# Optimization experiments

Measured on AMD Instinct MI355X. Metric: run time of the kernel, lower is better.

Reference implementation:

```python
import jax, jax.numpy as jnp
import numpy as np
import math

NUM_HEADS = 16
SEGMENT_SIZE = 256
DILATION_RATE = 2


def _hilbert_curve(n):
    if n == 1:
        return [(0, 0)]
    m = n // 2
    sub = _hilbert_curve(m)
    pts = [(y, x) for (x, y) in sub]
    pts += [(x, y + m) for (x, y) in sub]
    pts += [(x + m, y + m) for (x, y) in sub]
    pts += [(m - 1 - y + m, m - 1 - x) for (x, y) in sub]
    return pts


def generate_hilbert_curve_mapping(seq_len):
    grid = 2 ** int(math.ceil(math.log2(math.sqrt(seq_len))))
    pts = _hilbert_curve(grid)
    lin2hil = np.zeros(seq_len, dtype=np.int32)
    for h_idx, (x, y) in enumerate(pts[:seq_len]):
        lin = y * grid + x
        if lin < seq_len:
            lin2hil[lin] = h_idx
    return lin2hil


def setup_inputs() -> dict:
    key = jax.random.key(0)
    k1, k2, k3 = jax.random.split(key, 3)
    B, S, H = 1, 4096, 2048
    scale = H ** -0.5
    x = jax.random.normal(k1, (B, S, H), dtype=jnp.float32)
    w_qkv = jax.random.normal(k2, (3 * H, H), dtype=jnp.float32) * scale
    w_out = jax.random.normal(k3, (H, H), dtype=jnp.float32) * scale
    hilbert_map = jnp.asarray(generate_hilbert_curve_mapping(S))
    return {"x": x, "w_qkv": w_qkv, "w_out": w_out, "hilbert_map": hilbert_map}


def _kv_positions(S, seg, dil):
    # Union of per-segment dilated positions: seg_start + j*dil (< segment end).
    seg_starts = np.arange(0, S, seg)
    within = np.arange(0, seg, dil)
    return jnp.asarray((seg_starts[:, None] + within[None, :]).reshape(-1))


def reference(x, w_qkv, w_out, hilbert_map):
    B, S, H = x.shape
    nh = NUM_HEADS
    hd = H // nh
    qkv = x @ w_qkv.T                              # [B,S,3H]
    qkv = qkv.reshape(B, S, 3, nh, hd).transpose(2, 0, 3, 1, 4)  # [3,B,nh,S,hd]
    q, k, v = qkv[0], qkv[1], qkv[2]

    kv_pos = _kv_positions(S, SEGMENT_SIZE, DILATION_RATE)  # [Nk]
    gathered = hilbert_map[kv_pos]                 # Hilbert-mapped KV indices
    kg = k[:, :, gathered, :]                      # [B,nh,Nk,hd]
    vg = v[:, :, gathered, :]

    scale = 1.0 / jnp.sqrt(jnp.float32(hd))
    scores = jnp.einsum("bhmd,bhnd->bhmn", q, kg) * scale
    p = jax.nn.softmax(scores, axis=-1)
    acc = jnp.einsum("bhmn,bhnd->bhmd", p, vg)     # [B,nh,S,hd]

    # Scatter: out[:, :, hilbert_map[m], :] = acc[:, :, m, :]
    out = jnp.zeros_like(acc).at[:, :, hilbert_map, :].set(acc)
    out = out.transpose(0, 2, 1, 3).reshape(B, S, H)
    return out @ w_out.T
```

## Files before the change

### kernel.cpp

```cpp
#include <hip/hip_runtime.h>
#include <math.h>

#define S_LEN 4096
#define HID   2048
#define NH    16
#define HD    128
#define NKV   2048
#define KT    64
#define QBLK  256
#define NT    (NKV / KT)
#define QSCALE 0.12754103668587426f

typedef __attribute__((ext_vector_type(8))) _Float16 half8;
typedef __attribute__((ext_vector_type(4))) _Float16 half4;
typedef __attribute__((ext_vector_type(2))) __fp16 fp16x2;
typedef __attribute__((ext_vector_type(4))) float f32x4;
typedef __attribute__((ext_vector_type(16))) float f32x16;

#define GLB_AS __attribute__((address_space(1)))
#define LDS_AS __attribute__((address_space(3)))

#if __has_builtin(__builtin_amdgcn_exp2f)
#define EXP2(x) __builtin_amdgcn_exp2f(x)
#else
#define EXP2(x) exp2f(x)
#endif

__device__ __forceinline__ void gload16(const void* g, void* l) {
  __builtin_amdgcn_global_load_lds((GLB_AS const void*)g, (LDS_AS void*)l, 16, 0, 0);
}

__device__ __forceinline__ unsigned pkrtz(float a, float b) {
  union { fp16x2 h; unsigned u; } cv;
  cv.h = __builtin_amdgcn_cvt_pkrtz(a, b);
  return cv.u;
}

__global__ void k_build_idx(const int* __restrict__ hmap, int* __restrict__ gidx) {
  int i = blockIdx.x * 256 + threadIdx.x;
  if (i < NKV) gidx[i] = hmap[2 * i];
}

#define NX8  (S_LEN * HID / 8)
#define NW8  (3 * HID * HID / 8)
#define NO8  (HID * HID / 8)
__global__ void k_cvt_all(const float* __restrict__ x, const float* __restrict__ wq,
                          const float* __restrict__ wo, _Float16* __restrict__ x16,
                          _Float16* __restrict__ wq16, _Float16* __restrict__ wo16) {
  int i = blockIdx.x * 256 + threadIdx.x;
  const float* src; _Float16* dst; int j;
  if (i < NX8)            { src = x;  dst = x16;  j = i; }
  else if (i < NX8 + NW8) { src = wq; dst = wq16; j = i - NX8; }
  else                    { src = wo; dst = wo16; j = i - NX8 - NW8; }
  float4 a = ((const float4*)src)[2 * j];
  float4 b = ((const float4*)src)[2 * j + 1];
  half8 h;
  h[0] = (_Float16)a.x; h[1] = (_Float16)a.y; h[2] = (_Float16)a.z; h[3] = (_Float16)a.w;
  h[4] = (_Float16)b.x; h[5] = (_Float16)b.y; h[6] = (_Float16)b.z; h[7] = (_Float16)b.w;
  ((half8*)dst)[j] = h;
}

template<int MODE>
__global__ __launch_bounds__(256)
void k_gemm2(const _Float16* __restrict__ A, const _Float16* __restrict__ B,
             void* __restrict__ Cv, int M, int N, int K,
             const int* __restrict__ arow,
             char* __restrict__ kimg, char* __restrict__ vtimg)
{
  __shared__ __align__(16) char Asl[16384];
  __shared__ __align__(16) char Bsl[16384];
  const int tid = threadIdx.x;
  const int w = tid >> 6, lane = tid & 63;
  const int l15 = lane & 15, l4 = lane >> 4;
  const int m0 = blockIdx.y * 128, n0 = blockIdx.x * 128;
  const int wr = w >> 1, wc = w & 1;

  const int srow  = lane >> 3;
  const int kso   = ((lane & 7) ^ srow) * 8;
  const _Float16* Ap[4];
  const _Float16* Bp[4];
#pragma unroll
  for (int q = 0; q < 4; ++q) {
    int arel = m0 + 32 * w + 8 * q + srow;
    int ra = arow ? arow[arel] : arel;
    Ap[q] = A + (size_t)ra * K + kso;
    Bp[q] = B + (size_t)(n0 + 32 * w + 8 * q + srow) * K + kso;
  }

  f32x4 acc[4][4];
#pragma unroll
  for (int i = 0; i < 4; ++i)
#pragma unroll
    for (int j = 0; j < 4; ++j) acc[i][j] = (f32x4){0.f, 0.f, 0.f, 0.f};

#define STAGE_T(k0)                                                  \
  do {                                                               \
    _Pragma("unroll")                                                \
    for (int q = 0; q < 4; ++q) {                                    \
      gload16(Ap[q] + (k0), Asl + (4 * w + q) * 1024 + lane * 16);   \
      gload16(Bp[q] + (k0), Bsl + (4 * w + q) * 1024 + lane * 16);   \
    }                                                                \
  } while (0)

  STAGE_T(0);
  __syncthreads();

  const int nt = K >> 6;
  for (int t = 0; t < nt; ++t) {
    half8 af[4][2], bf[4][2];
#pragma unroll
    for (int mi = 0; mi < 4; ++mi) {
      int row = wr * 64 + mi * 16 + l15;
#pragma unroll
      for (int ks = 0; ks < 2; ++ks)
        af[mi][ks] = *(const half8*)(Asl + row * 128 + (((ks * 4 + l4) ^ (row & 7)) * 16));
    }
#pragma unroll
    for (int ni = 0; ni < 4; ++ni) {
      int row = wc * 64 + ni * 16 + l15;
#pragma unroll
      for (int ks = 0; ks < 2; ++ks)
        bf[ni][ks] = *(const half8*)(Bsl + row * 128 + (((ks * 4 + l4) ^ (row & 7)) * 16));
    }
    __syncthreads();
    if (t + 1 < nt) STAGE_T((t + 1) * 64);
    __builtin_amdgcn_s_setprio(1);
#pragma unroll
    for (int mi = 0; mi < 4; ++mi)
#pragma unroll
      for (int ni = 0; ni < 4; ++ni)
#pragma unroll
        for (int ks = 0; ks < 2; ++ks)
          acc[mi][ni] = __builtin_amdgcn_mfma_f32_16x16x32_f16(af[mi][ks], bf[ni][ks], acc[mi][ni], 0, 0, 0);
    __builtin_amdgcn_s_setprio(0);
    __syncthreads();
  }
#undef STAGE_T

  const int rbase = m0 + wr * 64 + l4 * 4;
  const int cbase = n0 + wc * 64 + l15;
#pragma unroll
  for (int mi = 0; mi < 4; ++mi)
#pragma unroll
    for (int ni = 0; ni < 4; ++ni)
#pragma unroll
      for (int e = 0; e < 4; ++e) {
        int row = rbase + mi * 16 + e;
        int col = cbase + ni * 16;
        if (MODE == 1) {
          ((float*)Cv)[(size_t)row * N + col] = acc[mi][ni][e];
        } else if (MODE == 0) {
          ((_Float16*)Cv)[(size_t)row * N + col] = (_Float16)acc[mi][ni][e];
        } else {
          _Float16 val = (_Float16)acc[mi][ni][e];
          int t = row >> 6, j = row & 63;
          if (col < HID) {
            int h = col >> 7, d = col & 127;
            int off = (h * 32 + t) * 16384 + ((j * 256 + 2 * d) ^ ((j & 7) << 4));
            *(_Float16*)(kimg + off) = val;
          } else {
            int nn = col - HID;
            int h = nn >> 7, d = nn & 127;
            int off = (h * 32 + t) * 16384 + ((d * 128 + 2 * j) ^ ((d & 7) << 4));
            *(_Float16*)(vtimg + off) = val;
          }
        }
      }
}

__global__ __launch_bounds__(512, 2)
void k_attn9(const _Float16* __restrict__ qmat, const char* __restrict__ kimg,
             const char* __restrict__ vtimg, const int* __restrict__ hmap,
             _Float16* __restrict__ att)
{
  extern __shared__ __align__(16) char lds[];
  const int tid = threadIdx.x;
  const int w = tid >> 6, lane = tid & 63;
  const int l31 = lane & 31;
  const bool hi = (lane >> 5) != 0;
  const int hib = hi ? 1 : 0;
  const int work = (blockIdx.x & 7) * 32 + (blockIdx.x >> 3);
  const int h  = work >> 4;
  const int q0 = (work & 15) * QBLK;

  half8 qf[8];
  {
    const int qrow = q0 + w * 32 + l31;
    const _Float16* qb = qmat + (size_t)qrow * HID + h * HD + hib * 8;
    const _Float16 qs = (_Float16)QSCALE;
#pragma unroll
    for (int dk = 0; dk < 8; ++dk) {
      half8 v = *(const half8*)(qb + 16 * dk);
#pragma unroll
      for (int q = 0; q < 8; ++q) v[q] *= qs;
      qf[dk] = v;
    }
  }

  const int swz = (l31 & 7) << 4;
  int koff[4], voff[4];
#pragma unroll
  for (int i = 0; i < 4; ++i) {
    koff[i] = l31 * 256 + ((i * 32 + hib * 16) ^ swz);
    voff[i] = 16384 + l31 * 128 + ((i * 32 + hib * 16) ^ swz);
  }

  const char* kbase = kimg  + (size_t)h * NT * 16384;
  const char* vbase = vtimg + (size_t)h * NT * 16384;

  f32x16 acc[4];
#pragma unroll
  for (int dt = 0; dt < 4; ++dt)
#pragma unroll
    for (int r = 0; r < 16; ++r) acc[dt][r] = 0.f;
  float lsum = 0.f;

#define STAGE(buf, t)                                                          \
  do {                                                                         \
    const char* ks_ = kbase + (size_t)(t) * 16384;                             \
    const char* vs_ = vbase + (size_t)(t) * 16384;                             \
    char* d_ = lds + (buf) * 32768;                                            \
    gload16(ks_ + w * 1024 + lane * 16,          d_ + w * 1024);               \
    gload16(ks_ + (8 + w) * 1024 + lane * 16,    d_ + (8 + w) * 1024);         \
    gload16(vs_ + w * 1024 + lane * 16,          d_ + 16384 + w * 1024);       \
    gload16(vs_ + (8 + w) * 1024 + lane * 16,    d_ + 16384 + (8 + w) * 1024); \
  } while (0)

#define SM_HALF(S, PPK)                                                        \
  do {                                                                         \
    float p_[16];                                                              \
    _Pragma("unroll")                                                          \
    for (int r = 0; r < 16; ++r) { p_[r] = EXP2((S)[r]); lsum += p_[r]; }      \
    _Pragma("unroll")                                                          \
    for (int rq = 0; rq < 4; ++rq)                                             \
      _Pragma("unroll")                                                        \
      for (int h2 = 0; h2 < 2; ++h2)                                           \
        PPK[rq][h2] = pkrtz(p_[4 * rq + 2 * h2], p_[4 * rq + 2 * h2 + 1]);     \
  } while (0)

#define PV_HALF(PPK, KSB, CUR)                                                 \
  do {                                                                         \
    _Pragma("unroll")                                                          \
    for (int k1 = 0; k1 < 2; ++k1) {                                           \
      unsigned send0 = hi ? PPK[2 * k1][0]     : PPK[2 * k1 + 1][0];           \
      unsigned send1 = hi ? PPK[2 * k1][1]     : PPK[2 * k1 + 1][1];           \
      unsigned recv0 = (unsigned)__shfl_xor((int)send0, 32);                   \
      unsigned recv1 = (unsigned)__shfl_xor((int)send1, 32);                   \
      unsigned self0 = hi ? PPK[2 * k1 + 1][0] : PPK[2 * k1][0];               \
      unsigned self1 = hi ? PPK[2 * k1 + 1][1] : PPK[2 * k1][1];               \
      union { unsigned u[4]; half8 hv; } pf;                                   \
      pf.u[0] = hi ? recv0 : self0;                                            \
      pf.u[1] = hi ? recv1 : self1;                                            \
      pf.u[2] = hi ? self0 : recv0;                                            \
      pf.u[3] = hi ? self1 : recv1;                                            \
      __builtin_amdgcn_s_setprio(1);                                           \
      _Pragma("unroll")                                                        \
      for (int dt = 0; dt < 4; ++dt) {                                         \
        half8 vf = *(const half8*)(lds + voff[(KSB) + k1] +                    \
                    ((CUR) * 32768 + dt * 4096));                              \
        acc[dt] = __builtin_amdgcn_mfma_f32_32x32x16_f16(vf, pf.hv, acc[dt], 0, 0, 0); \
      }                                                                        \
      __builtin_amdgcn_s_setprio(0);                                           \
    }                                                                          \
  } while (0)

#define QK_HALF(S, JT, CUR)                                                    \
  do {                                                                         \
    _Pragma("unroll")                                                          \
    for (int r = 0; r < 16; ++r) (S)[r] = 0.f;                                 \
    __builtin_amdgcn_s_setprio(1);                                             \
    _Pragma("unroll")                                                          \
    for (int dk = 0; dk < 8; ++dk) {                                           \
      half8 kf = *(const half8*)(lds + koff[dk & 3] +                          \
                  ((CUR) * 32768 + (JT) * 8192 + (dk >> 2) * 128));            \
      (S) = __builtin_amdgcn_mfma_f32_32x32x16_f16(kf, qf[dk], (S), 0, 0, 0);  \
    }                                                                          \
    __builtin_amdgcn_s_setprio(0);                                             \
  } while (0)

#define TILE(CUR, T)                                                           \
  do {                                                                         \
    if ((T) + 1 < NT) STAGE((CUR) ^ 1, (T) + 1);                               \
    f32x16 sA, sB;                                                             \
    QK_HALF(sA, 0, CUR);                                                       \
    QK_HALF(sB, 1, CUR);                                                       \
    unsigned PA[4][2], PB[4][2];                                               \
    SM_HALF(sA, PA);                         \
    PV_HALF(PA, 0, CUR);                                                       \
    SM_HALF(sB, PB);                    \
    PV_HALF(PB, 2, CUR);                                                       \
    asm volatile("s_waitcnt vmcnt(0)");                                        \
    __syncthreads();                                                           \
  } while (0)

  STAGE(0, 0);
  asm volatile("s_waitcnt vmcnt(0)");
  __syncthreads();

  for (int t = 0; t < NT; t += 2) {
    TILE(0, t);
    TILE(1, t + 1);
  }
#undef TILE
#undef QK_HALF
#undef PV_HALF
#undef SM_HALF
#undef STAGE

  float lt = lsum + __shfl_xor(lsum, 32);
  const float rl = 1.0f / lt;
  const int qrow = q0 + w * 32 + l31;
  const int srow = hmap[qrow];
  _Float16* ob = att + (size_t)srow * HID + h * HD;
#pragma unroll
  for (int dt = 0; dt < 4; ++dt)
#pragma unroll
    for (int rq = 0; rq < 4; ++rq) {
      const int d0 = dt * 32 + 8 * rq + 4 * hib;
      half4 o;
      o[0] = (_Float16)(acc[dt][4 * rq + 0] * rl);
      o[1] = (_Float16)(acc[dt][4 * rq + 1] * rl);
      o[2] = (_Float16)(acc[dt][4 * rq + 2] * rl);
      o[3] = (_Float16)(acc[dt][4 * rq + 3] * rl);
      *(half4*)(ob + d0) = o;
    }
}

extern "C" void kernel_launch(void* const* d_in, const int* in_sizes, int n_in,
                              void* d_out, int out_size, void* d_ws, size_t ws_size,
                              hipStream_t stream)
{
  const float* x     = (const float*)d_in[0];
  const float* w_qkv = (const float*)d_in[1];
  const float* w_out = (const float*)d_in[2];
  const int*   hmap  = (const int*)d_in[3];
  float* out = (float*)d_out;

  char* ws = (char*)d_ws;
  int* gidx = (int*)ws;                                          ws += 8192;
  _Float16* x16    = (_Float16*)ws;
  _Float16* att16  = (_Float16*)ws;                              ws += (size_t)S_LEN * HID * 2;
  _Float16* wqkv16 = (_Float16*)ws;                              ws += (size_t)3 * HID * HID * 2;
  _Float16* wout16 = (_Float16*)ws;                              ws += (size_t)HID * HID * 2;
  _Float16* q16    = (_Float16*)ws;                              ws += (size_t)S_LEN * HID * 2;
  char* kimg  = ws;                                              ws += (size_t)NH * NT * 16384;
  char* vtimg = ws;

  k_build_idx<<<8, 256, 0, stream>>>(hmap, gidx);
  k_cvt_all<<<(NX8 + NW8 + NO8 + 255) / 256, 256, 0, stream>>>(x, w_qkv, w_out,
                                                               x16, wqkv16, wout16);

  dim3 gq(HID / 128, S_LEN / 128);
  k_gemm2<0><<<gq, 256, 0, stream>>>(x16, wqkv16, q16, S_LEN, HID, HID, nullptr, nullptr, nullptr);
  dim3 gkv(2 * HID / 128, NKV / 128);
  k_gemm2<2><<<gkv, 256, 0, stream>>>(x16, wqkv16 + (size_t)HID * HID, nullptr,
                                      NKV, 2 * HID, HID, gidx, kimg, vtimg);

  k_attn9<<<NH * (S_LEN / QBLK), 512, 65536, stream>>>(q16, kimg, vtimg, hmap, att16);

  dim3 go(HID / 128, S_LEN / 128);
  k_gemm2<1><<<go, 256, 0, stream>>>(att16, wout16, out, S_LEN, HID, HID, nullptr, nullptr, nullptr);
}
```

Baseline: 217.9 us.

## Merge Q and KV projection GEMMs into one launch; halve attention query block

The Q projection and the gathered K/V projection GEMMs now run as a single 1024-block launch, with the block index choosing which part it computes. This removes one kernel launch and lets both parts share the GPU at once, filling the tail. The attention kernel drops from 256 to 128 query rows per block and from 512 to 256 threads, doubling the number of blocks to 512. The trade-off is that each K/V tile staged in LDS is reused by fewer query rows, so more K/V traffic is loaded per unit of work. The output GEMM becomes its own non-templated kernel.

```diff
diff --git a/kernel.cpp b/kernel.cpp
--- a/kernel.cpp
+++ b/kernel.cpp
@@ -7,7 +7,7 @@
 #define HD    128
 #define NKV   2048
 #define KT    64
-#define QBLK  256
+#define QBLK  128
 #define NT    (NKV / KT)
 #define QSCALE 0.12754103668587426f
 
@@ -60,20 +60,27 @@
   ((half8*)dst)[j] = h;
 }
 
-template<int MODE>
 __global__ __launch_bounds__(256)
-void k_gemm2(const _Float16* __restrict__ A, const _Float16* __restrict__ B,
-             void* __restrict__ Cv, int M, int N, int K,
-             const int* __restrict__ arow,
-             char* __restrict__ kimg, char* __restrict__ vtimg)
+void k_gemm_qkv(const _Float16* __restrict__ A, const _Float16* __restrict__ wqkv,
+                _Float16* __restrict__ q16, const int* __restrict__ gidx,
+                char* __restrict__ kimg, char* __restrict__ vtimg)
 {
   __shared__ __align__(16) char Asl[16384];
   __shared__ __align__(16) char Bsl[16384];
   const int tid = threadIdx.x;
   const int w = tid >> 6, lane = tid & 63;
   const int l15 = lane & 15, l4 = lane >> 4;
-  const int m0 = blockIdx.y * 128, n0 = blockIdx.x * 128;
   const int wr = w >> 1, wc = w & 1;
+  const int K = HID;
+
+  int b = blockIdx.x;
+  const bool qpart = b < 512;
+  int m0, n0, N;
+  const _Float16* B;
+  const int* arow;
+  if (qpart) { m0 = (b >> 4) * 128; n0 = (b & 15) * 128; N = HID; B = wqkv; arow = nullptr; }
+  else { b -= 512; m0 = (b >> 5) * 128; n0 = (b & 31) * 128; N = 2 * HID;
+         B = wqkv + (size_t)HID * HID; arow = gidx; }
 
   const int srow  = lane >> 3;
   const int kso   = ((lane & 7) ^ srow) * 8;
@@ -147,12 +154,10 @@
       for (int e = 0; e < 4; ++e) {
         int row = rbase + mi * 16 + e;
         int col = cbase + ni * 16;
-        if (MODE == 1) {
-          ((float*)Cv)[(size_t)row * N + col] = acc[mi][ni][e];
-        } else if (MODE == 0) {
-          ((_Float16*)Cv)[(size_t)row * N + col] = (_Float16)acc[mi][ni][e];
+        _Float16 val = (_Float16)acc[mi][ni][e];
+        if (qpart) {
+          q16[(size_t)row * HID + col] = val;
         } else {
-          _Float16 val = (_Float16)acc[mi][ni][e];
           int t = row >> 6, j = row & 63;
           if (col < HID) {
             int h = col >> 7, d = col & 127;
@@ -168,7 +173,91 @@
       }
 }
 
-__global__ __launch_bounds__(512, 2)
+__global__ __launch_bounds__(256)
+void k_gemm_out(const _Float16* __restrict__ A, const _Float16* __restrict__ B,
+                float* __restrict__ C, int M, int N, int K)
+{
+  __shared__ __align__(16) char Asl[16384];
+  __shared__ __align__(16) char Bsl[16384];
+  const int tid = threadIdx.x;
+  const int w = tid >> 6, lane = tid & 63;
+  const int l15 = lane & 15, l4 = lane >> 4;
+  const int m0 = blockIdx.y * 128, n0 = blockIdx.x * 128;
+  const int wr = w >> 1, wc = w & 1;
+
+  const int srow  = lane >> 3;
+  const int kso   = ((lane & 7) ^ srow) * 8;
+  const _Float16* Ap[4];
+  const _Float16* Bp[4];
+#pragma unroll
+  for (int q = 0; q < 4; ++q) {
+    int row = m0 + 32 * w + 8 * q + srow;
+    Ap[q] = A + (size_t)row * K + kso;
+    Bp[q] = B + (size_t)(n0 + 32 * w + 8 * q + srow) * K + kso;
+  }
+
+  f32x4 acc[4][4];
+#pragma unroll
+  for (int i = 0; i < 4; ++i)
+#pragma unroll
+    for (int j = 0; j < 4; ++j) acc[i][j] = (f32x4){0.f, 0.f, 0.f, 0.f};
+
+#define STAGE_T(k0)                                                  \
+  do {                                                               \
+    _Pragma("unroll")                                                \
+    for (int q = 0; q < 4; ++q) {                                    \
+      gload16(Ap[q] + (k0), Asl + (4 * w + q) * 1024 + lane * 16);   \
+      gload16(Bp[q] + (k0), Bsl + (4 * w + q) * 1024 + lane * 16);   \
+    }                                                                \
+  } while (0)
+
+  STAGE_T(0);
+  __syncthreads();
+
+  const int nt = K >> 6;
+  for (int t = 0; t < nt; ++t) {
+    half8 af[4][2], bf[4][2];
+#pragma unroll
+    for (int mi = 0; mi < 4; ++mi) {
+      int row = wr * 64 + mi * 16 + l15;
+#pragma unroll
+      for (int ks = 0; ks < 2; ++ks)
+        af[mi][ks] = *(const half8*)(Asl + row * 128 + (((ks * 4 + l4) ^ (row & 7)) * 16));
+    }
+#pragma unroll
+    for (int ni = 0; ni < 4; ++ni) {
+      int row = wc * 64 + ni * 16 + l15;
+#pragma unroll
+      for (int ks = 0; ks < 2; ++ks)
+        bf[ni][ks] = *(const half8*)(Bsl + row * 128 + (((ks * 4 + l4) ^ (row & 7)) * 16));
+    }
+    __syncthreads();
+    if (t + 1 < nt) STAGE_T((t + 1) * 64);
+    __builtin_amdgcn_s_setprio(1);
+#pragma unroll
+    for (int mi = 0; mi < 4; ++mi)
+#pragma unroll
+      for (int ni = 0; ni < 4; ++ni)
+#pragma unroll
+        for (int ks = 0; ks < 2; ++ks)
+          acc[mi][ni] = __builtin_amdgcn_mfma_f32_16x16x32_f16(af[mi][ks], bf[ni][ks], acc[mi][ni], 0, 0, 0);
+    __builtin_amdgcn_s_setprio(0);
+    __syncthreads();
+  }
+#undef STAGE_T
+
+  const int rbase = m0 + wr * 64 + l4 * 4;
+  const int cbase = n0 + wc * 64 + l15;
+#pragma unroll
+  for (int mi = 0; mi < 4; ++mi)
+#pragma unroll
+    for (int ni = 0; ni < 4; ++ni)
+#pragma unroll
+      for (int e = 0; e < 4; ++e)
+        C[(size_t)(rbase + mi * 16 + e) * N + cbase + ni * 16] = acc[mi][ni][e];
+}
+
+__global__ __launch_bounds__(256, 2)
 void k_attn9(const _Float16* __restrict__ qmat, const char* __restrict__ kimg,
              const char* __restrict__ vtimg, const int* __restrict__ hmap,
              _Float16* __restrict__ att)
@@ -179,9 +268,9 @@
   const int l31 = lane & 31;
   const bool hi = (lane >> 5) != 0;
   const int hib = hi ? 1 : 0;
-  const int work = (blockIdx.x & 7) * 32 + (blockIdx.x >> 3);
-  const int h  = work >> 4;
-  const int q0 = (work & 15) * QBLK;
+  const int work = (blockIdx.x & 7) * 64 + (blockIdx.x >> 3);
+  const int h  = work >> 5;
+  const int q0 = (work & 31) * QBLK;
 
   half8 qf[8];
   {
@@ -220,10 +309,12 @@
     const char* ks_ = kbase + (size_t)(t) * 16384;                             \
     const char* vs_ = vbase + (size_t)(t) * 16384;                             \
     char* d_ = lds + (buf) * 32768;                                            \
-    gload16(ks_ + w * 1024 + lane * 16,          d_ + w * 1024);               \
-    gload16(ks_ + (8 + w) * 1024 + lane * 16,    d_ + (8 + w) * 1024);         \
-    gload16(vs_ + w * 1024 + lane * 16,          d_ + 16384 + w * 1024);       \
-    gload16(vs_ + (8 + w) * 1024 + lane * 16,    d_ + 16384 + (8 + w) * 1024); \
+    _Pragma("unroll")                                                          \
+    for (int g = 0; g < 4; ++g) {                                              \
+      gload16(ks_ + (w + 4 * g) * 1024 + lane * 16, d_ + (w + 4 * g) * 1024);  \
+      gload16(vs_ + (w + 4 * g) * 1024 + lane * 16,                            \
+              d_ + 16384 + (w + 4 * g) * 1024);                                \
+    }                                                                          \
   } while (0)
 
 #define SM_HALF(S, PPK)                                                        \
@@ -285,9 +376,9 @@
     QK_HALF(sA, 0, CUR);                                                       \
     QK_HALF(sB, 1, CUR);                                                       \
     unsigned PA[4][2], PB[4][2];                                               \
-    SM_HALF(sA, PA);                         \
+    SM_HALF(sA, PA);                                                           \
     PV_HALF(PA, 0, CUR);                                                       \
-    SM_HALF(sB, PB);                    \
+    SM_HALF(sB, PB);                                                           \
     PV_HALF(PB, 2, CUR);                                                       \
     asm volatile("s_waitcnt vmcnt(0)");                                        \
     __syncthreads();                                                           \
@@ -350,14 +441,10 @@
   k_cvt_all<<<(NX8 + NW8 + NO8 + 255) / 256, 256, 0, stream>>>(x, w_qkv, w_out,
                                                                x16, wqkv16, wout16);
 
-  dim3 gq(HID / 128, S_LEN / 128);
-  k_gemm2<0><<<gq, 256, 0, stream>>>(x16, wqkv16, q16, S_LEN, HID, HID, nullptr, nullptr, nullptr);
-  dim3 gkv(2 * HID / 128, NKV / 128);
-  k_gemm2<2><<<gkv, 256, 0, stream>>>(x16, wqkv16 + (size_t)HID * HID, nullptr,
-                                      NKV, 2 * HID, HID, gidx, kimg, vtimg);
-
-  k_attn9<<<NH * (S_LEN / QBLK), 512, 65536, stream>>>(q16, kimg, vtimg, hmap, att16);
+  k_gemm_qkv<<<1024, 256, 0, stream>>>(x16, wqkv16, q16, gidx, kimg, vtimg);
+
+  k_attn9<<<NH * (S_LEN / QBLK), 256, 65536, stream>>>(q16, kimg, vtimg, hmap, att16);
 
   dim3 go(HID / 128, S_LEN / 128);
-  k_gemm2<1><<<go, 256, 0, stream>>>(att16, wout16, out, S_LEN, HID, HID, nullptr, nullptr, nullptr);
-}
+  k_gemm_out<<<go, 256, 0, stream>>>(att16, wout16, out, S_LEN, HID, HID);
+}
```

Result: slower. 224.5 us (+3.0%).

## Fuse Q and KV projections into one 256x256-tile, 8-wave pipelined GEMM

Applied to the files above, without the earlier changes.

Replaces the two separate 128x128 GEMM launches for Q and gathered K/V with a single launch of 256 blocks using 256x256 tiles, 512 threads and a 128KB double-buffered LDS. The main loop is split into eight quarter-phases that interleave fragment loads, async global-to-LDS staging and MFMA work, with raw barriers and partial vmcnt waits. The goal is more data reuse per tile, fewer launches and better load/compute overlap. In exchange LDS per block is much larger, so occupancy drops, and the hand-written wait and barrier schedule adds correctness risk. The output GEMM is kept as a separate copy of the old kernel.

```diff
diff --git a/kernel.cpp b/kernel.cpp
--- a/kernel.cpp
+++ b/kernel.cpp
@@ -60,100 +60,141 @@
   ((half8*)dst)[j] = h;
 }
 
-template<int MODE>
-__global__ __launch_bounds__(256)
-void k_gemm2(const _Float16* __restrict__ A, const _Float16* __restrict__ B,
-             void* __restrict__ Cv, int M, int N, int K,
-             const int* __restrict__ arow,
-             char* __restrict__ kimg, char* __restrict__ vtimg)
+__global__ __launch_bounds__(512, 2)
+void k_gemm_qkv8(const _Float16* __restrict__ A, const _Float16* __restrict__ wqkv,
+                 _Float16* __restrict__ q16, const int* __restrict__ gidx,
+                 char* __restrict__ kimg, char* __restrict__ vtimg)
 {
-  __shared__ __align__(16) char Asl[16384];
-  __shared__ __align__(16) char Bsl[16384];
+  extern __shared__ __align__(16) char lds[];
   const int tid = threadIdx.x;
   const int w = tid >> 6, lane = tid & 63;
   const int l15 = lane & 15, l4 = lane >> 4;
-  const int m0 = blockIdx.y * 128, n0 = blockIdx.x * 128;
-  const int wr = w >> 1, wc = w & 1;
-
-  const int srow  = lane >> 3;
-  const int kso   = ((lane & 7) ^ srow) * 8;
-  const _Float16* Ap[4];
-  const _Float16* Bp[4];
-#pragma unroll
-  for (int q = 0; q < 4; ++q) {
-    int arel = m0 + 32 * w + 8 * q + srow;
-    int ra = arow ? arow[arel] : arel;
-    Ap[q] = A + (size_t)ra * K + kso;
-    Bp[q] = B + (size_t)(n0 + 32 * w + 8 * q + srow) * K + kso;
-  }
-
-  f32x4 acc[4][4];
-#pragma unroll
-  for (int i = 0; i < 4; ++i)
+  const int wr = w >> 2, wc = w & 3;
+  const int K = HID;
+
+  const int bid = (blockIdx.x & 7) * 32 + (blockIdx.x >> 3);
+  const bool qpart = bid < 128;
+  int m0, n0;
+  const _Float16* B;
+  if (qpart) { int b = bid;       m0 = (b >> 3) * 256; n0 = (b & 7) * 256;  B = wqkv; }
+  else       { int b = bid - 128; m0 = (b >> 4) * 256; n0 = (b & 15) * 256; B = wqkv + (size_t)HID * HID; }
+
+  const int r8 = lane >> 3;
+  const int sl = (lane & 7) ^ r8;
+  const _Float16* ApA[2][2];
+  const _Float16* BpB[2][2];
+#pragma unroll
+  for (int mh = 0; mh < 2; ++mh)
+#pragma unroll
+    for (int L = 0; L < 2; ++L) {
+      int rel = L * 128 + mh * 64 + w * 8 + r8;
+      int grow = qpart ? (m0 + rel) : gidx[m0 + rel];
+      ApA[mh][L] = A + (size_t)grow * K + sl * 8;
+    }
+#pragma unroll
+  for (int nh = 0; nh < 2; ++nh)
+#pragma unroll
+    for (int L = 0; L < 2; ++L) {
+      int row = n0 + (L * 2 + (w >> 2)) * 64 + nh * 32 + (w & 3) * 8 + r8;
+      BpB[nh][L] = B + (size_t)row * K + sl * 8;
+    }
+
+  const int sw0 = (l4 ^ (l15 & 7)) * 16;
+  const int sw1 = ((4 + l4) ^ (l15 & 7)) * 16;
+  const int rofs = l15 * 128;
+
+  f32x4 acc[8][4];
+#pragma unroll
+  for (int i = 0; i < 8; ++i)
 #pragma unroll
     for (int j = 0; j < 4; ++j) acc[i][j] = (f32x4){0.f, 0.f, 0.f, 0.f};
-
-#define STAGE_T(k0)                                                  \
-  do {                                                               \
-    _Pragma("unroll")                                                \
-    for (int q = 0; q < 4; ++q) {                                    \
-      gload16(Ap[q] + (k0), Asl + (4 * w + q) * 1024 + lane * 16);   \
-      gload16(Bp[q] + (k0), Bsl + (4 * w + q) * 1024 + lane * 16);   \
-    }                                                                \
-  } while (0)
-
-  STAGE_T(0);
-  __syncthreads();
-
-  const int nt = K >> 6;
-  for (int t = 0; t < nt; ++t) {
-    half8 af[4][2], bf[4][2];
-#pragma unroll
-    for (int mi = 0; mi < 4; ++mi) {
-      int row = wr * 64 + mi * 16 + l15;
-#pragma unroll
-      for (int ks = 0; ks < 2; ++ks)
-        af[mi][ks] = *(const half8*)(Asl + row * 128 + (((ks * 4 + l4) ^ (row & 7)) * 16));
-    }
-#pragma unroll
-    for (int ni = 0; ni < 4; ++ni) {
-      int row = wc * 64 + ni * 16 + l15;
-#pragma unroll
-      for (int ks = 0; ks < 2; ++ks)
-        bf[ni][ks] = *(const half8*)(Bsl + row * 128 + (((ks * 4 + l4) ^ (row & 7)) * 16));
-    }
-    __syncthreads();
-    if (t + 1 < nt) STAGE_T((t + 1) * 64);
-    __builtin_amdgcn_s_setprio(1);
-#pragma unroll
-    for (int mi = 0; mi < 4; ++mi)
-#pragma unroll
-      for (int ni = 0; ni < 4; ++ni)
-#pragma unroll
-        for (int ks = 0; ks < 2; ++ks)
-          acc[mi][ni] = __builtin_amdgcn_mfma_f32_16x16x32_f16(af[mi][ks], bf[ni][ks], acc[mi][ni], 0, 0, 0);
-    __builtin_amdgcn_s_setprio(0);
-    __syncthreads();
-  }
-#undef STAGE_T
-
-  const int rbase = m0 + wr * 64 + l4 * 4;
-  const int cbase = n0 + wc * 64 + l15;
-#pragma unroll
-  for (int mi = 0; mi < 4; ++mi)
-#pragma unroll
-    for (int ni = 0; ni < 4; ++ni)
+  half8 af[4][2], bf[2][2];
+
+#define STG_A(MH, BUF, T)                                                       \
+  do {                                                                          \
+    gload16(ApA[MH][0] + (T) * 64, lds + (BUF)*65536 + (MH)*16384 + w * 1024);  \
+    gload16(ApA[MH][1] + (T) * 64, lds + (BUF)*65536 + (MH)*16384 + 8192 + w * 1024); \
+  } while (0)
+#define STG_B(NH, BUF, T)                                                       \
+  do {                                                                          \
+    gload16(BpB[NH][0] + (T) * 64, lds + (BUF)*65536 + 32768 + (NH)*16384 + w * 1024); \
+    gload16(BpB[NH][1] + (T) * 64, lds + (BUF)*65536 + 32768 + (NH)*16384 + 8192 + w * 1024); \
+  } while (0)
+
+#define PH(BUF, MH, NH, LA, LB, STG, WAITS)                                     \
+  do {                                                                          \
+    if (LA) {                                                                   \
+      _Pragma("unroll")                                                         \
+      for (int j = 0; j < 4; ++j) {                                             \
+        af[j][0] = *(const half8*)(lds + (BUF)*65536 + (MH)*16384 + wr * 8192 + j * 2048 + rofs + sw0); \
+        af[j][1] = *(const half8*)(lds + (BUF)*65536 + (MH)*16384 + wr * 8192 + j * 2048 + rofs + sw1); \
+      }                                                                         \
+    }                                                                           \
+    if (LB) {                                                                   \
+      _Pragma("unroll")                                                         \
+      for (int jn = 0; jn < 2; ++jn) {                                          \
+        bf[jn][0] = *(const half8*)(lds + (BUF)*65536 + 32768 + (NH)*16384 + wc * 4096 + jn * 2048 + rofs + sw0); \
+        bf[jn][1] = *(const half8*)(lds + (BUF)*65536 + 32768 + (NH)*16384 + wc * 4096 + jn * 2048 + rofs + sw1); \
+      }                                                                         \
+    }                                                                           \
+    STG;                                                                        \
+    __builtin_amdgcn_s_barrier();                                               \
+    __builtin_amdgcn_s_setprio(1);                                              \
+    _Pragma("unroll")                                                           \
+    for (int j = 0; j < 4; ++j)                                                 \
+      _Pragma("unroll")                                                         \
+      for (int jn = 0; jn < 2; ++jn)                                            \
+        _Pragma("unroll")                                                       \
+        for (int ks = 0; ks < 2; ++ks)                                          \
+          acc[(MH)*4 + j][(NH)*2 + jn] = __builtin_amdgcn_mfma_f32_16x16x32_f16( \
+              af[j][ks], bf[jn][ks], acc[(MH)*4 + j][(NH)*2 + jn], 0, 0, 0);    \
+    __builtin_amdgcn_s_setprio(0);                                              \
+    WAITS;                                                                      \
+    __builtin_amdgcn_s_barrier();                                               \
+  } while (0)
+
+  STG_A(0, 0, 0); STG_B(1, 0, 0); STG_A(1, 0, 0); STG_B(0, 0, 0);
+  STG_A(0, 1, 1); STG_B(1, 1, 1);
+  asm volatile("s_waitcnt vmcnt(4)");
+  __builtin_amdgcn_s_barrier();
+
+  for (int i = 0; i < 15; ++i) {
+    const int T1 = 2 * i + 1, T2 = 2 * i + 2, T3 = 2 * i + 3;
+    PH(0, 0, 0, 1, 1, STG_A(1, 1, T1), (void)0);
+    PH(0, 0, 1, 0, 1, STG_B(0, 1, T1), (void)0);
+    PH(0, 1, 1, 1, 0, STG_A(0, 0, T2), (void)0);
+    PH(0, 1, 0, 0, 1, STG_B(1, 0, T2), asm volatile("s_waitcnt vmcnt(4)"));
+    PH(1, 0, 0, 1, 1, STG_A(1, 0, T2), (void)0);
+    PH(1, 0, 1, 0, 1, STG_B(0, 0, T2), (void)0);
+    PH(1, 1, 1, 1, 0, STG_A(0, 1, T3), (void)0);
+    PH(1, 1, 0, 0, 1, STG_B(1, 1, T3), asm volatile("s_waitcnt vmcnt(4)"));
+  }
+  PH(0, 0, 0, 1, 1, STG_A(1, 1, 31), (void)0);
+  PH(0, 0, 1, 0, 1, STG_B(0, 1, 31), (void)0);
+  PH(0, 1, 1, 1, 0, (void)0, (void)0);
+  PH(0, 1, 0, 0, 1, (void)0, asm volatile("s_waitcnt vmcnt(0)"));
+  PH(1, 0, 0, 1, 1, (void)0, (void)0);
+  PH(1, 0, 1, 0, 1, (void)0, (void)0);
+  PH(1, 1, 1, 1, 0, (void)0, (void)0);
+  PH(1, 1, 0, 0, 1, (void)0, (void)0);
+#undef PH
+#undef STG_A
+#undef STG_B
+
+#pragma unroll
+  for (int mf = 0; mf < 8; ++mf)
+#pragma unroll
+    for (int nf = 0; nf < 4; ++nf)
 #pragma unroll
       for (int e = 0; e < 4; ++e) {
-        int row = rbase + mi * 16 + e;
-        int col = cbase + ni * 16;
-        if (MODE == 1) {
-          ((float*)Cv)[(size_t)row * N + col] = acc[mi][ni][e];
-        } else if (MODE == 0) {
-          ((_Float16*)Cv)[(size_t)row * N + col] = (_Float16)acc[mi][ni][e];
+        int row = m0 + wr * 128 + mf * 16 + l4 * 4 + e;
+        int col = n0 + wc * 64 + nf * 16 + l15;
+        _Float16 val = (_Float16)acc[mf][nf][e];
+        if (qpart) {
+          q16[(size_t)row * HID + col] = val;
         } else {
-          _Float16 val = (_Float16)acc[mi][ni][e];
-          int t = row >> 6, j = row & 63;
+          int r = row - m0 + m0;
+          int t = r >> 6, j = r & 63;
           if (col < HID) {
             int h = col >> 7, d = col & 127;
             int off = (h * 32 + t) * 16384 + ((j * 256 + 2 * d) ^ ((j & 7) << 4));
@@ -166,6 +207,90 @@
           }
         }
       }
+}
+
+__global__ __launch_bounds__(256)
+void k_gemm_out(const _Float16* __restrict__ A, const _Float16* __restrict__ B,
+                float* __restrict__ C, int M, int N, int K)
+{
+  __shared__ __align__(16) char Asl[16384];
+  __shared__ __align__(16) char Bsl[16384];
+  const int tid = threadIdx.x;
+  const int w = tid >> 6, lane = tid & 63;
+  const int l15 = lane & 15, l4 = lane >> 4;
+  const int m0 = blockIdx.y * 128, n0 = blockIdx.x * 128;
+  const int wr = w >> 1, wc = w & 1;
+
+  const int srow  = lane >> 3;
+  const int kso   = ((lane & 7) ^ srow) * 8;
+  const _Float16* Ap[4];
+  const _Float16* Bp[4];
+#pragma unroll
+  for (int q = 0; q < 4; ++q) {
+    int row = m0 + 32 * w + 8 * q + srow;
+    Ap[q] = A + (size_t)row * K + kso;
+    Bp[q] = B + (size_t)(n0 + 32 * w + 8 * q + srow) * K + kso;
+  }
+
+  f32x4 acc[4][4];
+#pragma unroll
+  for (int i = 0; i < 4; ++i)
+#pragma unroll
+    for (int j = 0; j < 4; ++j) acc[i][j] = (f32x4){0.f, 0.f, 0.f, 0.f};
+
+#define STAGE_T(k0)                                                  \
+  do {                                                               \
+    _Pragma("unroll")                                                \
+    for (int q = 0; q < 4; ++q) {                                    \
+      gload16(Ap[q] + (k0), Asl + (4 * w + q) * 1024 + lane * 16);   \
+      gload16(Bp[q] + (k0), Bsl + (4 * w + q) * 1024 + lane * 16);   \
+    }                                                                \
+  } while (0)
+
+  STAGE_T(0);
+  __syncthreads();
+
+  const int nt = K >> 6;
+  for (int t = 0; t < nt; ++t) {
+    half8 af[4][2], bf[4][2];
+#pragma unroll
+    for (int mi = 0; mi < 4; ++mi) {
+      int row = wr * 64 + mi * 16 + l15;
+#pragma unroll
+      for (int ks = 0; ks < 2; ++ks)
+        af[mi][ks] = *(const half8*)(Asl + row * 128 + (((ks * 4 + l4) ^ (row & 7)) * 16));
+    }
+#pragma unroll
+    for (int ni = 0; ni < 4; ++ni) {
+      int row = wc * 64 + ni * 16 + l15;
+#pragma unroll
+      for (int ks = 0; ks < 2; ++ks)
+        bf[ni][ks] = *(const half8*)(Bsl + row * 128 + (((ks * 4 + l4) ^ (row & 7)) * 16));
+    }
+    __syncthreads();
+    if (t + 1 < nt) STAGE_T((t + 1) * 64);
+    __builtin_amdgcn_s_setprio(1);
+#pragma unroll
+    for (int mi = 0; mi < 4; ++mi)
+#pragma unroll
+      for (int ni = 0; ni < 4; ++ni)
+#pragma unroll
+        for (int ks = 0; ks < 2; ++ks)
+          acc[mi][ni] = __builtin_amdgcn_mfma_f32_16x16x32_f16(af[mi][ks], bf[ni][ks], acc[mi][ni], 0, 0, 0);
+    __builtin_amdgcn_s_setprio(0);
+    __syncthreads();
+  }
+#undef STAGE_T
+
+  const int rbase = m0 + wr * 64 + l4 * 4;
+  const int cbase = n0 + wc * 64 + l15;
+#pragma unroll
+  for (int mi = 0; mi < 4; ++mi)
+#pragma unroll
+    for (int ni = 0; ni < 4; ++ni)
+#pragma unroll
+      for (int e = 0; e < 4; ++e)
+        C[(size_t)(rbase + mi * 16 + e) * N + cbase + ni * 16] = acc[mi][ni][e];
 }
 
 __global__ __launch_bounds__(512, 2)
@@ -285,9 +410,9 @@
     QK_HALF(sA, 0, CUR);                                                       \
     QK_HALF(sB, 1, CUR);                                                       \
     unsigned PA[4][2], PB[4][2];                                               \
-    SM_HALF(sA, PA);                         \
+    SM_HALF(sA, PA);                                                           \
     PV_HALF(PA, 0, CUR);                                                       \
-    SM_HALF(sB, PB);                    \
+    SM_HALF(sB, PB);                                                           \
     PV_HALF(PB, 2, CUR);                                                       \
     asm volatile("s_waitcnt vmcnt(0)");                                        \
     __syncthreads();                                                           \
@@ -350,14 +475,10 @@
   k_cvt_all<<<(NX8 + NW8 + NO8 + 255) / 256, 256, 0, stream>>>(x, w_qkv, w_out,
                                                                x16, wqkv16, wout16);
 
-  dim3 gq(HID / 128, S_LEN / 128);
-  k_gemm2<0><<<gq, 256, 0, stream>>>(x16, wqkv16, q16, S_LEN, HID, HID, nullptr, nullptr, nullptr);
-  dim3 gkv(2 * HID / 128, NKV / 128);
-  k_gemm2<2><<<gkv, 256, 0, stream>>>(x16, wqkv16 + (size_t)HID * HID, nullptr,
-                                      NKV, 2 * HID, HID, gidx, kimg, vtimg);
+  k_gemm_qkv8<<<256, 512, 131072, stream>>>(x16, wqkv16, q16, gidx, kimg, vtimg);
 
   k_attn9<<<NH * (S_LEN / QBLK), 512, 65536, stream>>>(q16, kimg, vtimg, hmap, att16);
 
   dim3 go(HID / 128, S_LEN / 128);
-  k_gemm2<1><<<go, 256, 0, stream>>>(att16, wout16, out, S_LEN, HID, HID, nullptr, nullptr, nullptr);
-}
+  k_gemm_out<<<go, 256, 0, stream>>>(att16, wout16, out, S_LEN, HID, HID);
+}
```

Measured after the change: 213.5 us. -2.0%, faster.
